# Kernel tuning notes

Hardware: AMD Instinct MI355X
Metric: run time of the kernel (lower is better)

## Reference

```python
import jax, jax.numpy as jnp
import numpy as np

B, T = 16, 4096
H = 1024            # rnn_dims
HALF = H // 2       # half_rnn_dims
FC = 1024           # fc_dims
FEAT, AUX = 80, 64
NC = 256            # n_classes
D_IN = FEAT + AUX + 3


def setup_inputs() -> dict:
    key = jax.random.key(0)
    ks = jax.random.split(key, 20)
    s = 0.02
    inp = {
        "x": jax.random.normal(ks[0], (B, T, 3), jnp.float32),
        "feat": jax.random.normal(ks[1], (B, T, FEAT), jnp.float32),
        "aux1": jax.random.normal(ks[2], (B, T, AUX), jnp.float32),
        "aux2": jax.random.normal(ks[3], (B, T, AUX), jnp.float32),
        "aux3": jax.random.normal(ks[4], (B, T, AUX), jnp.float32),
        # GRU parameters (PyTorch layout: [3*H, in] with r,z,n gate order)
        "w_ih": jax.random.normal(ks[5], (3 * H, D_IN), jnp.float32) * s,
        "w_hh": jax.random.normal(ks[6], (3 * H, H), jnp.float32) * s,
        "b_ih": jax.random.normal(ks[7], (3 * H,), jnp.float32) * s,
        "b_hh": jax.random.normal(ks[8], (3 * H,), jnp.float32) * s,
        # coarse head
        "w1": jax.random.normal(ks[9], (FC, HALF + AUX), jnp.float32) * s,
        "b1": jax.random.normal(ks[10], (FC,), jnp.float32) * s,
        "w2": jax.random.normal(ks[11], (NC, FC), jnp.float32) * s,
        "b2": jax.random.normal(ks[12], (NC,), jnp.float32) * s,
        # fine head
        "w3": jax.random.normal(ks[13], (FC, HALF + AUX), jnp.float32) * s,
        "b3": jax.random.normal(ks[14], (FC,), jnp.float32) * s,
        "w4": jax.random.normal(ks[15], (NC, FC), jnp.float32) * s,
        "b4": jax.random.normal(ks[16], (NC,), jnp.float32) * s,
    }
    return inp


def _gru(inp_btd, w_ih, w_hh, b_ih, b_hh):
    # Precompute input projection for all timesteps: [B,T,3H]
    xp = jnp.einsum("btd,gd->btg", inp_btd, w_ih) + b_ih
    xp = jnp.transpose(xp, (1, 0, 2))  # [T,B,3H]
    h0 = jnp.zeros((inp_btd.shape[0], H), inp_btd.dtype)

    def step(h, xt):
        gh = h @ w_hh.T + b_hh                      # [B,3H]
        xr, xz, xn = jnp.split(xt, 3, axis=1)
        hr, hz, hn = jnp.split(gh, 3, axis=1)
        r = jax.nn.sigmoid(xr + hr)
        z = jax.nn.sigmoid(xz + hz)
        n = jnp.tanh(xn + r * hn)
        h_new = (1.0 - z) * n + z * h
        return h_new, h_new

    _, hs = jax.lax.scan(step, h0, xp)              # [T,B,H]
    return jnp.transpose(hs, (1, 0, 2))             # [B,T,H]


def reference(x, feat, aux1, aux2, aux3, w_ih, w_hh, b_ih, b_hh,
              w1, b1, w2, b2, w3, b3, w4, b4):
    inp = jnp.concatenate([feat, aux1, x], axis=2)  # [B,T,FEAT+AUX+3]
    h = _gru(inp, w_ih, w_hh, b_ih, b_hh)           # [B,T,H]
    h_c, h_f = h[..., :HALF], h[..., HALF:]
    o_c = jax.nn.relu(jnp.concatenate([h_c, aux2], axis=2) @ w1.T + b1)
    p_c = jax.nn.log_softmax(o_c @ w2.T + b2, axis=2)
    o_f = jax.nn.relu(jnp.concatenate([h_f, aux3], axis=2) @ w3.T + b3)
    p_f = jax.nn.log_softmax(o_f @ w4.T + b4, axis=2)
    return (p_c, p_f)
```

## Files before the change

kernel.cpp:

```cpp
#include <hip/hip_runtime.h>
#include <hip/hip_bf16.h>

#define TSTEPS 4096
#define BATCH 16
#define HID 1024
#define DIN 147
#define KIN 160
#define KC  (HID + KIN)
#define NWG 64
#define NCLS 256
#define FCN 1024
#define KFC 576

typedef __attribute__((ext_vector_type(8))) short short8;
typedef __attribute__((ext_vector_type(4))) float floatx4;

__device__ __forceinline__ unsigned short f2b(float f) {
  __hip_bfloat16 h = __float2bfloat16(f);
  return *reinterpret_cast<unsigned short*>(&h);
}

#define GLOAD_LDS16(g, l) __builtin_amdgcn_global_load_lds( \
    (const __attribute__((address_space(1))) void*)(g), \
    (__attribute__((address_space(3))) void*)(l), 16, 0, 0)


__global__ void k_pack(const float* __restrict__ x, const float* __restrict__ feat,
                       const float* __restrict__ aux1, const float* __restrict__ aux2,
                       const float* __restrict__ aux3,
                       unsigned short* __restrict__ Xg, unsigned short* __restrict__ H,
                       unsigned short* __restrict__ a2b, unsigned short* __restrict__ a3b,
                       unsigned int* __restrict__ flags) {
  const int t = blockIdx.x;
  const int tid = threadIdx.x;
  for (int i = tid; i < BATCH * KIN; i += 256) {
    int b = i / KIN, k = i - b * KIN;
    float v = 0.f;
    if (k < 80)       v = feat[((size_t)b * TSTEPS + t) * 80 + k];
    else if (k < 144) v = aux1[((size_t)b * TSTEPS + t) * 64 + (k - 80)];
    else if (k < 147) v = x[((size_t)b * TSTEPS + t) * 3 + (k - 144)];
    Xg[((size_t)t * BATCH + b) * KIN + k] = f2b(v);
  }
  for (int i = tid; i < BATCH * 64; i += 256) {
    int b = i >> 6, k = i & 63;
    a2b[(size_t)t * (BATCH * 64) + i] = f2b(aux2[((size_t)b * TSTEPS + t) * 64 + k]);
    a3b[(size_t)t * (BATCH * 64) + i] = f2b(aux3[((size_t)b * TSTEPS + t) * 64 + k]);
  }
  if (t == 0) {
    for (int i = tid; i < BATCH * HID; i += 256) H[i] = 0;
    for (int i = tid; i < TSTEPS; i += 256) flags[i] = 0u;
  }
}

__global__ void k_wconv(const float* __restrict__ w_ih, const float* __restrict__ w_hh,
                        const float* __restrict__ w1, const float* __restrict__ w2,
                        const float* __restrict__ w3, const float* __restrict__ w4,
                        unsigned short* __restrict__ Wc,
                        unsigned short* __restrict__ w1b, unsigned short* __restrict__ w2b,
                        unsigned short* __restrict__ w3b, unsigned short* __restrict__ w4b) {
  const int bid = blockIdx.x, tid = threadIdx.x;
  if (bid < 3072) {
    const int row = bid;
    for (int k = tid; k < KC; k += 256) {
      float v = 0.f;
      if (k < HID) v = w_hh[(size_t)row * HID + k];
      else if (k < HID + DIN) v = w_ih[(size_t)row * DIN + (k - HID)];
      Wc[(size_t)row * KC + k] = f2b(v);
    }
  } else if (bid < 4096) {
    const int row = bid - 3072;
    for (int k = tid; k < KFC; k += 256) w1b[(size_t)row * KFC + k] = f2b(w1[(size_t)row * KFC + k]);
  } else if (bid < 4352) {
    const int row = bid - 4096;
    for (int k = tid; k < FCN; k += 256) w2b[(size_t)row * FCN + k] = f2b(w2[(size_t)row * FCN + k]);
  } else if (bid < 5376) {
    const int row = bid - 4352;
    for (int k = tid; k < KFC; k += 256) w3b[(size_t)row * KFC + k] = f2b(w3[(size_t)row * KFC + k]);
  } else {
    const int row = bid - 5376;
    for (int k = tid; k < FCN; k += 256) w4b[(size_t)row * FCN + k] = f2b(w4[(size_t)row * FCN + k]);
  }
}

__launch_bounds__(192, 1)
__global__ void k_gru(const unsigned short* __restrict__ Wc,
                      const float* __restrict__ b_ih, const float* __restrict__ b_hh,
                      const unsigned short* __restrict__ Xg,
                      unsigned short* __restrict__ H,
                      unsigned int* __restrict__ flags) {
  const int tid  = threadIdx.x;
  const int wg   = blockIdx.x;
  const int wave = tid >> 6;
  const int gate = wave;
  const int lane = tid & 63;
  const int cn   = lane & 15;
  const int quad = lane >> 4;
  const int c0   = wg * 16;
  const int grow = gate * HID + c0 + cn;

  short8 wf[37];
  {
    const short8* wptr = reinterpret_cast<const short8*>(Wc + (size_t)grow * KC);
#pragma unroll
    for (int ks = 0; ks < 37; ks++) wf[ks] = wptr[ks * 4 + quad];
  }
  const float bih = b_ih[grow];
  const float bhh = b_hh[grow];
  const float brz = bih + bhh;

  float hprev[4] = {0.f, 0.f, 0.f, 0.f};

  __shared__ unsigned short lh[16 * 1024];
  __shared__ float lds_z[256];
  __shared__ float lds_hn[256];
  __shared__ float lds_xn[256];
  __shared__ __align__(16) unsigned lds_hout[128];

  const int swz = (cn & 7) << 3;

  for (int t = 0; t < TSTEPS; t++) {
    floatx4 accx = {0.f, 0.f, 0.f, 0.f};
    {
      const short8* xptr = reinterpret_cast<const short8*>(Xg + ((size_t)t * BATCH + cn) * KIN);
      short8 ax[5];
#pragma unroll
      for (int ks = 0; ks < 5; ks++) ax[ks] = xptr[ks * 4 + quad];
#pragma unroll
      for (int ks = 0; ks < 5; ks++)
        accx = __builtin_amdgcn_mfma_f32_16x16x32_bf16(ax[ks], wf[32 + ks], accx, 0, 0, 0);
    }

    if (wave == 1) {
      const unsigned need = (unsigned)t;
      for (;;) {
        unsigned f = __hip_atomic_load(&flags[lane * 4], __ATOMIC_RELAXED,
                                       __HIP_MEMORY_SCOPE_SYSTEM);
        if (__ballot(f >= need) == ~0ull) break;
      }
      const char* Ht = reinterpret_cast<const char*>(H + (size_t)t * BATCH * HID);
      char* lbase = reinterpret_cast<char*>(lh);
#pragma unroll
      for (int i = 0; i < 32; i++) {
        const int d  = (i << 10) + (lane << 4);
        const int r  = d >> 11;
        const int lb = (d & 2047) ^ ((r & 7) << 4);
        const char* g = Ht + ((lb >> 5) << 9) + (r << 5) + (lb & 31);
        GLOAD_LDS16(g, lbase + (i << 10));
      }
      asm volatile("s_waitcnt vmcnt(0)" ::: "memory");
    }
    asm volatile("" ::: "memory");
    __syncthreads();

    floatx4 acc0 = {0.f, 0.f, 0.f, 0.f};
    floatx4 acc1 = {0.f, 0.f, 0.f, 0.f};
    {
      const int rb = cn * 1024;
#pragma unroll
      for (int ks = 0; ks < 32; ks += 2) {
        short8 a0 = *reinterpret_cast<const short8*>(&lh[rb + (((ks    ) * 32 + quad * 8) ^ swz)]);
        short8 a1 = *reinterpret_cast<const short8*>(&lh[rb + (((ks + 1) * 32 + quad * 8) ^ swz)]);
        acc0 = __builtin_amdgcn_mfma_f32_16x16x32_bf16(a0, wf[ks],     acc0, 0, 0, 0);
        acc1 = __builtin_amdgcn_mfma_f32_16x16x32_bf16(a1, wf[ks + 1], acc1, 0, 0, 0);
      }
    }

    float rr[4];
    if (gate == 0) {
#pragma unroll
      for (int j = 0; j < 4; j++) {
        float g = acc0[j] + acc1[j] + accx[j] + brz;
        rr[j] = __builtin_amdgcn_rcpf(1.f + __expf(-g));
      }
    } else if (gate == 1) {
#pragma unroll
      for (int j = 0; j < 4; j++) {
        float g = acc0[j] + acc1[j] + accx[j] + brz;
        lds_z[(quad * 4 + j) * 16 + cn] = __builtin_amdgcn_rcpf(1.f + __expf(-g));
      }
    } else {
#pragma unroll
      for (int j = 0; j < 4; j++) {
        int idx = (quad * 4 + j) * 16 + cn;
        lds_hn[idx] = acc0[j] + acc1[j] + bhh;
        lds_xn[idx] = accx[j] + bih;
      }
    }
    __syncthreads();

    if (gate == 0) {
#pragma unroll
      for (int j = 0; j < 4; j++) {
        int idx = (quad * 4 + j) * 16 + cn;
        float z = lds_z[idx];
        float a = lds_xn[idx] + rr[j] * lds_hn[idx];
        float e2 = __expf(2.f * a);
        float n = 1.f - 2.f * __builtin_amdgcn_rcpf(e2 + 1.f);
        float h = (1.f - z) * n + z * hprev[j];
        hprev[j] = h;
        unsigned hv = (unsigned)f2b(h);
        unsigned pv = __shfl_xor(hv, 1);
        if ((cn & 1) == 0)
          lds_hout[(quad * 4 + j) * 8 + (cn >> 1)] = hv | (pv << 16);
      }
      unsigned long long v8 = reinterpret_cast<unsigned long long*>(lds_hout)[lane];
      unsigned long long* dst =
          reinterpret_cast<unsigned long long*>(H + (size_t)(t + 1) * BATCH * HID + wg * 256) + lane;
      __hip_atomic_store(dst, v8, __ATOMIC_RELAXED, __HIP_MEMORY_SCOPE_SYSTEM);
      asm volatile("s_waitcnt vmcnt(0)" ::: "memory");
      if (lane == 0)
        __hip_atomic_store(&flags[wg * 4], (unsigned)(t + 1), __ATOMIC_RELAXED,
                           __HIP_MEMORY_SCOPE_SYSTEM);
    }
  }
}

__launch_bounds__(256, 2)
__global__ void k_fc(const unsigned short* __restrict__ H,
                     const unsigned short* __restrict__ a2b, const unsigned short* __restrict__ a3b,
                     const unsigned short* __restrict__ w1b, const unsigned short* __restrict__ w2b,
                     const unsigned short* __restrict__ w3b, const unsigned short* __restrict__ w4b,
                     const float* __restrict__ b1, const float* __restrict__ b2,
                     const float* __restrict__ b3, const float* __restrict__ b4,
                     float* __restrict__ out) {
  const int br = blockIdx.x & 1;
  const int t  = blockIdx.x >> 1;
  const unsigned short* wAp = br ? w3b : w1b;
  const unsigned short* wBp = br ? w4b : w2b;
  const float* bA = br ? b3 : b1;
  const float* bB = br ? b4 : b2;
  const unsigned short* aux = br ? a3b : a2b;
  float* outp = out + (size_t)br * BATCH * TSTEPS * NCLS;

  __shared__ __align__(16) unsigned char smemU[16 * 584 * 2];
  __shared__ __align__(16) unsigned short lO[16][1032];
  unsigned short (*lA)[584] = reinterpret_cast<unsigned short(*)[584]>(smemU);
  float (*lZ)[260] = reinterpret_cast<float(*)[260]>(smemU);

  const int tid  = threadIdx.x;
  const int wave = tid >> 6;
  const int lane = tid & 63;
  const int cn   = lane & 15;
  const int quad = lane >> 4;

  {
    const unsigned short* hb = H + (size_t)(t + 1) * BATCH * HID;
    for (int cid = tid; cid < 16 * 72; cid += 256) {
      int r = cid / 72, off = (cid - r * 72) * 8;
      uint4 v;
      if (off < 512)
        v = *reinterpret_cast<const uint4*>(hb + ((size_t)(br * 32 + (off >> 4))) * 256 + r * 16 + (off & 15));
      else
        v = *reinterpret_cast<const uint4*>(aux + ((size_t)t * 16 + r) * 64 + (off - 512));
      *reinterpret_cast<uint4*>(&lA[r][off]) = v;
    }
  }
  __syncthreads();

  {
    short8 af[18];
#pragma unroll
    for (int ks = 0; ks < 18; ks++)
      af[ks] = *reinterpret_cast<const short8*>(&lA[cn][ks * 32 + quad * 8]);

    for (int nt = 0; nt < 16; nt++) {
      const int colg = wave * 256 + nt * 16 + cn;
      const short8* bptr = reinterpret_cast<const short8*>(wAp + (size_t)colg * KFC);
      floatx4 acc = {0.f, 0.f, 0.f, 0.f};
#pragma unroll
      for (int ks = 0; ks < 18; ks++)
        acc = __builtin_amdgcn_mfma_f32_16x16x32_bf16(af[ks], bptr[ks * 4 + quad], acc, 0, 0, 0);
      const float bias = bA[colg];
#pragma unroll
      for (int j = 0; j < 4; j++) {
        float v = acc[j] + bias;
        v = v > 0.f ? v : 0.f;
        lO[quad * 4 + j][colg] = f2b(v);
      }
    }
  }
  __syncthreads();

  {
    short8 of[32];
#pragma unroll
    for (int ks = 0; ks < 32; ks++)
      of[ks] = *reinterpret_cast<const short8*>(&lO[cn][ks * 32 + quad * 8]);

    for (int nt = 0; nt < 4; nt++) {
      const int cls = wave * 64 + nt * 16 + cn;
      const short8* bptr = reinterpret_cast<const short8*>(wBp + (size_t)cls * FCN);
      floatx4 acc = {0.f, 0.f, 0.f, 0.f};
#pragma unroll
      for (int ks = 0; ks < 32; ks++)
        acc = __builtin_amdgcn_mfma_f32_16x16x32_bf16(of[ks], bptr[ks * 4 + quad], acc, 0, 0, 0);
      const float bias = bB[cls];
#pragma unroll
      for (int j = 0; j < 4; j++)
        lZ[quad * 4 + j][cls] = acc[j] + bias;
    }
  }
  __syncthreads();

  {
    const int r = tid >> 4, j = tid & 15;
    float vals[16];
    float m = -3.4e38f;
#pragma unroll
    for (int i = 0; i < 16; i++) {
      float v = lZ[r][j + 16 * i];
      vals[i] = v;
      m = fmaxf(m, v);
    }
#pragma unroll
    for (int s = 8; s > 0; s >>= 1) m = fmaxf(m, __shfl_xor(m, s, 16));
    float ssum = 0.f;
#pragma unroll
    for (int i = 0; i < 16; i++) ssum += __expf(vals[i] - m);
#pragma unroll
    for (int s = 8; s > 0; s >>= 1) ssum += __shfl_xor(ssum, s, 16);
    const float lse = m + __logf(ssum);
    float* orow = outp + ((size_t)r * TSTEPS + t) * NCLS;
#pragma unroll
    for (int i = 0; i < 16; i++) orow[j + 16 * i] = vals[i] - lse;
  }
}

extern "C" void kernel_launch(void* const* d_in, const int* in_sizes, int n_in,
                              void* d_out, int out_size, void* d_ws, size_t ws_size,
                              hipStream_t stream) {
  const float* x    = (const float*)d_in[0];
  const float* feat = (const float*)d_in[1];
  const float* aux1 = (const float*)d_in[2];
  const float* aux2 = (const float*)d_in[3];
  const float* aux3 = (const float*)d_in[4];
  const float* w_ih = (const float*)d_in[5];
  const float* w_hh = (const float*)d_in[6];
  const float* b_ih = (const float*)d_in[7];
  const float* b_hh = (const float*)d_in[8];
  const float* w1   = (const float*)d_in[9];
  const float* b1   = (const float*)d_in[10];
  const float* w2   = (const float*)d_in[11];
  const float* b2   = (const float*)d_in[12];
  const float* w3   = (const float*)d_in[13];
  const float* b3   = (const float*)d_in[14];
  const float* w4   = (const float*)d_in[15];
  const float* b4   = (const float*)d_in[16];
  float* out = (float*)d_out;

  char* p = (char*)d_ws;
  unsigned short* H   = (unsigned short*)p; p += (size_t)(TSTEPS + 1) * BATCH * HID * 2;
  unsigned short* Xg  = (unsigned short*)p; p += (size_t)TSTEPS * BATCH * KIN * 2;
  unsigned int*  flags = (unsigned int*)p;  p += (size_t)TSTEPS * 4;
  unsigned short* Wc  = (unsigned short*)p; p += (size_t)3072 * KC * 2;
  unsigned short* w1b = (unsigned short*)p; p += (size_t)1024 * KFC * 2;
  unsigned short* w2b = (unsigned short*)p; p += (size_t)256 * FCN * 2;
  unsigned short* w3b = (unsigned short*)p; p += (size_t)1024 * KFC * 2;
  unsigned short* w4b = (unsigned short*)p; p += (size_t)256 * FCN * 2;
  unsigned short* a2b = (unsigned short*)p; p += (size_t)TSTEPS * BATCH * 64 * 2;
  unsigned short* a3b = (unsigned short*)p; p += (size_t)TSTEPS * BATCH * 64 * 2;

  if ((size_t)(p - (char*)d_ws) > ws_size) return;

  k_pack<<<TSTEPS, 256, 0, stream>>>(x, feat, aux1, aux2, aux3, Xg, H, a2b, a3b, flags);
  k_wconv<<<5632, 256, 0, stream>>>(w_ih, w_hh, w1, w2, w3, w4, Wc, w1b, w2b, w3b, w4b);
  k_gru<<<NWG, 192, 0, stream>>>(Wc, b_ih, b_hh, Xg, H, flags);
  k_fc<<<TSTEPS * 2, 256, 0, stream>>>(H, a2b, a3b, w1b, w2b, w3b, w4b, b1, b2, b3, b4, out);
}
```

Baseline: 13.81 ms.

## Fuse FC heads into persistent GRU kernel to overlap with recurrence

The FC/log-softmax heads move into the persistent GRU kernel as 160 extra consumer workgroups. Each one polls the per-workgroup step flags and processes timesteps as soon as the hidden state for that step is published, so the head computation overlaps the serial recurrence instead of running afterwards in a separate launch. The flag layout is also compacted from a stride of four to contiguous entries. The risk is that consumer blocks compete with the latency-critical GRU blocks for memory bandwidth and L2, and they rely on all 224 blocks being co-resident.

Result: slower. 15.79 ms (+14.3%).

```diff
diff --git a/kernel.cpp b/kernel.cpp
--- a/kernel.cpp
+++ b/kernel.cpp
@@ -8,6 +8,7 @@
 #define KIN 160
 #define KC  (HID + KIN)
 #define NWG 64
+#define NFC 160
 #define NCLS 256
 #define FCN 1024
 #define KFC 576
@@ -48,7 +49,7 @@
   }
   if (t == 0) {
     for (int i = tid; i < BATCH * HID; i += 256) H[i] = 0;
-    for (int i = tid; i < TSTEPS; i += 256) flags[i] = 0u;
+    for (int i = tid; i < 256; i += 256) flags[i] = 0u;
   }
 }
 
@@ -87,155 +88,14 @@
                       const float* __restrict__ b_ih, const float* __restrict__ b_hh,
                       const unsigned short* __restrict__ Xg,
                       unsigned short* __restrict__ H,
-                      unsigned int* __restrict__ flags) {
-  const int tid  = threadIdx.x;
-  const int wg   = blockIdx.x;
-  const int wave = tid >> 6;
-  const int gate = wave;
-  const int lane = tid & 63;
-  const int cn   = lane & 15;
-  const int quad = lane >> 4;
-  const int c0   = wg * 16;
-  const int grow = gate * HID + c0 + cn;
-
-  short8 wf[37];
-  {
-    const short8* wptr = reinterpret_cast<const short8*>(Wc + (size_t)grow * KC);
-#pragma unroll
-    for (int ks = 0; ks < 37; ks++) wf[ks] = wptr[ks * 4 + quad];
-  }
-  const float bih = b_ih[grow];
-  const float bhh = b_hh[grow];
-  const float brz = bih + bhh;
-
-  float hprev[4] = {0.f, 0.f, 0.f, 0.f};
-
-  __shared__ unsigned short lh[16 * 1024];
-  __shared__ float lds_z[256];
-  __shared__ float lds_hn[256];
-  __shared__ float lds_xn[256];
-  __shared__ __align__(16) unsigned lds_hout[128];
-
-  const int swz = (cn & 7) << 3;
-
-  for (int t = 0; t < TSTEPS; t++) {
-    floatx4 accx = {0.f, 0.f, 0.f, 0.f};
-    {
-      const short8* xptr = reinterpret_cast<const short8*>(Xg + ((size_t)t * BATCH + cn) * KIN);
-      short8 ax[5];
-#pragma unroll
-      for (int ks = 0; ks < 5; ks++) ax[ks] = xptr[ks * 4 + quad];
-#pragma unroll
-      for (int ks = 0; ks < 5; ks++)
-        accx = __builtin_amdgcn_mfma_f32_16x16x32_bf16(ax[ks], wf[32 + ks], accx, 0, 0, 0);
-    }
-
-    if (wave == 1) {
-      const unsigned need = (unsigned)t;
-      for (;;) {
-        unsigned f = __hip_atomic_load(&flags[lane * 4], __ATOMIC_RELAXED,
-                                       __HIP_MEMORY_SCOPE_SYSTEM);
-        if (__ballot(f >= need) == ~0ull) break;
-      }
-      const char* Ht = reinterpret_cast<const char*>(H + (size_t)t * BATCH * HID);
-      char* lbase = reinterpret_cast<char*>(lh);
-#pragma unroll
-      for (int i = 0; i < 32; i++) {
-        const int d  = (i << 10) + (lane << 4);
-        const int r  = d >> 11;
-        const int lb = (d & 2047) ^ ((r & 7) << 4);
-        const char* g = Ht + ((lb >> 5) << 9) + (r << 5) + (lb & 31);
-        GLOAD_LDS16(g, lbase + (i << 10));
-      }
-      asm volatile("s_waitcnt vmcnt(0)" ::: "memory");
-    }
-    asm volatile("" ::: "memory");
-    __syncthreads();
-
-    floatx4 acc0 = {0.f, 0.f, 0.f, 0.f};
-    floatx4 acc1 = {0.f, 0.f, 0.f, 0.f};
-    {
-      const int rb = cn * 1024;
-#pragma unroll
-      for (int ks = 0; ks < 32; ks += 2) {
-        short8 a0 = *reinterpret_cast<const short8*>(&lh[rb + (((ks    ) * 32 + quad * 8) ^ swz)]);
-        short8 a1 = *reinterpret_cast<const short8*>(&lh[rb + (((ks + 1) * 32 + quad * 8) ^ swz)]);
-        acc0 = __builtin_amdgcn_mfma_f32_16x16x32_bf16(a0, wf[ks],     acc0, 0, 0, 0);
-        acc1 = __builtin_amdgcn_mfma_f32_16x16x32_bf16(a1, wf[ks + 1], acc1, 0, 0, 0);
-      }
-    }
-
-    float rr[4];
-    if (gate == 0) {
-#pragma unroll
-      for (int j = 0; j < 4; j++) {
-        float g = acc0[j] + acc1[j] + accx[j] + brz;
-        rr[j] = __builtin_amdgcn_rcpf(1.f + __expf(-g));
-      }
-    } else if (gate == 1) {
-#pragma unroll
-      for (int j = 0; j < 4; j++) {
-        float g = acc0[j] + acc1[j] + accx[j] + brz;
-        lds_z[(quad * 4 + j) * 16 + cn] = __builtin_amdgcn_rcpf(1.f + __expf(-g));
-      }
-    } else {
-#pragma unroll
-      for (int j = 0; j < 4; j++) {
-        int idx = (quad * 4 + j) * 16 + cn;
-        lds_hn[idx] = acc0[j] + acc1[j] + bhh;
-        lds_xn[idx] = accx[j] + bih;
-      }
-    }
-    __syncthreads();
-
-    if (gate == 0) {
-#pragma unroll
-      for (int j = 0; j < 4; j++) {
-        int idx = (quad * 4 + j) * 16 + cn;
-        float z = lds_z[idx];
-        float a = lds_xn[idx] + rr[j] * lds_hn[idx];
-        float e2 = __expf(2.f * a);
-        float n = 1.f - 2.f * __builtin_amdgcn_rcpf(e2 + 1.f);
-        float h = (1.f - z) * n + z * hprev[j];
-        hprev[j] = h;
-        unsigned hv = (unsigned)f2b(h);
-        unsigned pv = __shfl_xor(hv, 1);
-        if ((cn & 1) == 0)
-          lds_hout[(quad * 4 + j) * 8 + (cn >> 1)] = hv | (pv << 16);
-      }
-      unsigned long long v8 = reinterpret_cast<unsigned long long*>(lds_hout)[lane];
-      unsigned long long* dst =
-          reinterpret_cast<unsigned long long*>(H + (size_t)(t + 1) * BATCH * HID + wg * 256) + lane;
-      __hip_atomic_store(dst, v8, __ATOMIC_RELAXED, __HIP_MEMORY_SCOPE_SYSTEM);
-      asm volatile("s_waitcnt vmcnt(0)" ::: "memory");
-      if (lane == 0)
-        __hip_atomic_store(&flags[wg * 4], (unsigned)(t + 1), __ATOMIC_RELAXED,
-                           __HIP_MEMORY_SCOPE_SYSTEM);
-    }
-  }
-}
-
-__launch_bounds__(256, 2)
-__global__ void k_fc(const unsigned short* __restrict__ H,
-                     const unsigned short* __restrict__ a2b, const unsigned short* __restrict__ a3b,
-                     const unsigned short* __restrict__ w1b, const unsigned short* __restrict__ w2b,
-                     const unsigned short* __restrict__ w3b, const unsigned short* __restrict__ w4b,
-                     const float* __restrict__ b1, const float* __restrict__ b2,
-                     const float* __restrict__ b3, const float* __restrict__ b4,
-                     float* __restrict__ out) {
-  const int br = blockIdx.x & 1;
-  const int t  = blockIdx.x >> 1;
-  const unsigned short* wAp = br ? w3b : w1b;
-  const unsigned short* wBp = br ? w4b : w2b;
-  const float* bA = br ? b3 : b1;
-  const float* bB = br ? b4 : b2;
-  const unsigned short* aux = br ? a3b : a2b;
-  float* outp = out + (size_t)br * BATCH * TSTEPS * NCLS;
-
-  __shared__ __align__(16) unsigned char smemU[16 * 584 * 2];
-  __shared__ __align__(16) unsigned short lO[16][1032];
-  unsigned short (*lA)[584] = reinterpret_cast<unsigned short(*)[584]>(smemU);
-  float (*lZ)[260] = reinterpret_cast<float(*)[260]>(smemU);
+                      unsigned int* __restrict__ flags,
+                      const unsigned short* __restrict__ a2b, const unsigned short* __restrict__ a3b,
+                      const unsigned short* __restrict__ w1b, const unsigned short* __restrict__ w2b,
+                      const unsigned short* __restrict__ w3b, const unsigned short* __restrict__ w4b,
+                      const float* __restrict__ b1, const float* __restrict__ b2,
+                      const float* __restrict__ b3, const float* __restrict__ b4,
+                      float* __restrict__ out) {
+  __shared__ __align__(16) unsigned char smem[51712];
 
   const int tid  = threadIdx.x;
   const int wave = tid >> 6;
@@ -243,86 +103,235 @@
   const int cn   = lane & 15;
   const int quad = lane >> 4;
 
-  {
-    const unsigned short* hb = H + (size_t)(t + 1) * BATCH * HID;
-    for (int cid = tid; cid < 16 * 72; cid += 256) {
-      int r = cid / 72, off = (cid - r * 72) * 8;
-      uint4 v;
-      if (off < 512)
-        v = *reinterpret_cast<const uint4*>(hb + ((size_t)(br * 32 + (off >> 4))) * 256 + r * 16 + (off & 15));
-      else
-        v = *reinterpret_cast<const uint4*>(aux + ((size_t)t * 16 + r) * 64 + (off - 512));
-      *reinterpret_cast<uint4*>(&lA[r][off]) = v;
+  if (blockIdx.x < NWG) {
+    const int wg   = blockIdx.x;
+    const int gate = wave;
+    const int grow = gate * HID + wg * 16 + cn;
+
+    unsigned short* lh = reinterpret_cast<unsigned short*>(smem);
+    float* lds_z  = reinterpret_cast<float*>(smem + 32768);
+    float* lds_hn = reinterpret_cast<float*>(smem + 32768 + 1024);
+    float* lds_xn = reinterpret_cast<float*>(smem + 32768 + 2048);
+    unsigned* lds_hout = reinterpret_cast<unsigned*>(smem + 32768 + 3072);
+
+    short8 wf[37];
+    {
+      const short8* wptr = reinterpret_cast<const short8*>(Wc + (size_t)grow * KC);
+#pragma unroll
+      for (int ks = 0; ks < 37; ks++) wf[ks] = wptr[ks * 4 + quad];
     }
-  }
-  __syncthreads();
-
-  {
-    short8 af[18];
-#pragma unroll
-    for (int ks = 0; ks < 18; ks++)
-      af[ks] = *reinterpret_cast<const short8*>(&lA[cn][ks * 32 + quad * 8]);
-
-    for (int nt = 0; nt < 16; nt++) {
-      const int colg = wave * 256 + nt * 16 + cn;
-      const short8* bptr = reinterpret_cast<const short8*>(wAp + (size_t)colg * KFC);
-      floatx4 acc = {0.f, 0.f, 0.f, 0.f};
-#pragma unroll
-      for (int ks = 0; ks < 18; ks++)
-        acc = __builtin_amdgcn_mfma_f32_16x16x32_bf16(af[ks], bptr[ks * 4 + quad], acc, 0, 0, 0);
-      const float bias = bA[colg];
-#pragma unroll
-      for (int j = 0; j < 4; j++) {
-        float v = acc[j] + bias;
-        v = v > 0.f ? v : 0.f;
-        lO[quad * 4 + j][colg] = f2b(v);
+    const float bih = b_ih[grow];
+    const float bhh = b_hh[grow];
+    const float brz = bih + bhh;
+
+    float hprev[4] = {0.f, 0.f, 0.f, 0.f};
+    const int swz = (cn & 7) << 3;
+
+    for (int t = 0; t < TSTEPS; t++) {
+      floatx4 accx = {0.f, 0.f, 0.f, 0.f};
+      {
+        const short8* xptr = reinterpret_cast<const short8*>(Xg + ((size_t)t * BATCH + cn) * KIN);
+        short8 ax[5];
+#pragma unroll
+        for (int ks = 0; ks < 5; ks++) ax[ks] = xptr[ks * 4 + quad];
+#pragma unroll
+        for (int ks = 0; ks < 5; ks++)
+          accx = __builtin_amdgcn_mfma_f32_16x16x32_bf16(ax[ks], wf[32 + ks], accx, 0, 0, 0);
+      }
+
+      if (wave == 1) {
+        const unsigned need = (unsigned)t;
+        for (;;) {
+          unsigned f = __hip_atomic_load(&flags[lane], __ATOMIC_RELAXED,
+                                         __HIP_MEMORY_SCOPE_SYSTEM);
+          if (__ballot(f >= need) == ~0ull) break;
+        }
+        const char* Ht = reinterpret_cast<const char*>(H + (size_t)t * BATCH * HID);
+        char* lbase = reinterpret_cast<char*>(lh);
+#pragma unroll
+        for (int i = 0; i < 32; i++) {
+          const int d  = (i << 10) + (lane << 4);
+          const int r  = d >> 11;
+          const int lb = (d & 2047) ^ ((r & 7) << 4);
+          const char* g = Ht + ((lb >> 5) << 9) + (r << 5) + (lb & 31);
+          GLOAD_LDS16(g, lbase + (i << 10));
+        }
+        asm volatile("s_waitcnt vmcnt(0)" ::: "memory");
+      }
+      asm volatile("" ::: "memory");
+      __syncthreads();
+
+      floatx4 acc0 = {0.f, 0.f, 0.f, 0.f};
+      floatx4 acc1 = {0.f, 0.f, 0.f, 0.f};
+      {
+        const int rb = cn * 1024;
+#pragma unroll
+        for (int ks = 0; ks < 32; ks += 2) {
+          short8 a0 = *reinterpret_cast<const short8*>(&lh[rb + (((ks    ) * 32 + quad * 8) ^ swz)]);
+          short8 a1 = *reinterpret_cast<const short8*>(&lh[rb + (((ks + 1) * 32 + quad * 8) ^ swz)]);
+          acc0 = __builtin_amdgcn_mfma_f32_16x16x32_bf16(a0, wf[ks],     acc0, 0, 0, 0);
+          acc1 = __builtin_amdgcn_mfma_f32_16x16x32_bf16(a1, wf[ks + 1], acc1, 0, 0, 0);
+        }
+      }
+
+      float rr[4];
+      if (gate == 0) {
+#pragma unroll
+        for (int j = 0; j < 4; j++) {
+          float g = acc0[j] + acc1[j] + accx[j] + brz;
+          rr[j] = __builtin_amdgcn_rcpf(1.f + __expf(-g));
+        }
+      } else if (gate == 1) {
+#pragma unroll
+        for (int j = 0; j < 4; j++) {
+          float g = acc0[j] + acc1[j] + accx[j] + brz;
+          lds_z[(quad * 4 + j) * 16 + cn] = __builtin_amdgcn_rcpf(1.f + __expf(-g));
+        }
+      } else {
+#pragma unroll
+        for (int j = 0; j < 4; j++) {
+          int idx = (quad * 4 + j) * 16 + cn;
+          lds_hn[idx] = acc0[j] + acc1[j] + bhh;
+          lds_xn[idx] = accx[j] + bih;
+        }
+      }
+      __syncthreads();
+
+      if (gate == 0) {
+#pragma unroll
+        for (int j = 0; j < 4; j++) {
+          int idx = (quad * 4 + j) * 16 + cn;
+          float z = lds_z[idx];
+          float a = lds_xn[idx] + rr[j] * lds_hn[idx];
+          float e2 = __expf(2.f * a);
+          float n = 1.f - 2.f * __builtin_amdgcn_rcpf(e2 + 1.f);
+          float h = (1.f - z) * n + z * hprev[j];
+          hprev[j] = h;
+          unsigned hv = (unsigned)f2b(h);
+          unsigned pv = __shfl_xor(hv, 1);
+          if ((cn & 1) == 0)
+            lds_hout[(quad * 4 + j) * 8 + (cn >> 1)] = hv | (pv << 16);
+        }
+        unsigned long long v8 = reinterpret_cast<unsigned long long*>(lds_hout)[lane];
+        unsigned long long* dst =
+            reinterpret_cast<unsigned long long*>(H + (size_t)(t + 1) * BATCH * HID + wg * 256) + lane;
+        __hip_atomic_store(dst, v8, __ATOMIC_RELAXED, __HIP_MEMORY_SCOPE_SYSTEM);
+        asm volatile("s_waitcnt vmcnt(0)" ::: "memory");
+        if (lane == 0)
+          __hip_atomic_store(&flags[wg], (unsigned)(t + 1), __ATOMIC_RELAXED,
+                             __HIP_MEMORY_SCOPE_SYSTEM);
       }
     }
-  }
-  __syncthreads();
-
-  {
-    short8 of[32];
-#pragma unroll
-    for (int ks = 0; ks < 32; ks++)
-      of[ks] = *reinterpret_cast<const short8*>(&lO[cn][ks * 32 + quad * 8]);
-
-    for (int nt = 0; nt < 4; nt++) {
-      const int cls = wave * 64 + nt * 16 + cn;
-      const short8* bptr = reinterpret_cast<const short8*>(wBp + (size_t)cls * FCN);
-      floatx4 acc = {0.f, 0.f, 0.f, 0.f};
-#pragma unroll
-      for (int ks = 0; ks < 32; ks++)
-        acc = __builtin_amdgcn_mfma_f32_16x16x32_bf16(of[ks], bptr[ks * 4 + quad], acc, 0, 0, 0);
-      const float bias = bB[cls];
-#pragma unroll
-      for (int j = 0; j < 4; j++)
-        lZ[quad * 4 + j][cls] = acc[j] + bias;
+  } else {
+    const int w = blockIdx.x - NWG;
+    unsigned short (*lA)[584] = reinterpret_cast<unsigned short(*)[584]>(smem);
+    float (*lZ)[260] = reinterpret_cast<float(*)[260]>(smem);
+    unsigned short (*lO)[1032] = reinterpret_cast<unsigned short(*)[1032]>(smem + 18688);
+
+    for (int idx = w; idx < TSTEPS * 2; idx += NFC) {
+      const int t  = idx >> 1;
+      const int br = idx & 1;
+      const unsigned short* wAp = br ? w3b : w1b;
+      const unsigned short* wBp = br ? w4b : w2b;
+      const float* bA = br ? b3 : b1;
+      const float* bB = br ? b4 : b2;
+      const unsigned short* aux = br ? a3b : a2b;
+      float* outp = out + (size_t)br * BATCH * TSTEPS * NCLS;
+
+      if (wave == 0) {
+        const unsigned need = (unsigned)(t + 1);
+        for (;;) {
+          unsigned f = __hip_atomic_load(&flags[lane], __ATOMIC_RELAXED,
+                                         __HIP_MEMORY_SCOPE_SYSTEM);
+          if (__ballot(f >= need) == ~0ull) break;
+          __builtin_amdgcn_s_sleep(32);
+        }
+      }
+      __syncthreads();
+
+      {
+        const unsigned short* hb = H + (size_t)(t + 1) * BATCH * HID;
+        for (int cid = tid; cid < 16 * 72; cid += 192) {
+          int r = cid / 72, off = (cid - r * 72) * 8;
+          uint4 v;
+          if (off < 512)
+            v = *reinterpret_cast<const uint4*>(hb + ((size_t)(br * 32 + (off >> 4))) * 256 + r * 16 + (off & 15));
+          else
+            v = *reinterpret_cast<const uint4*>(aux + ((size_t)t * 16 + r) * 64 + (off - 512));
+          *reinterpret_cast<uint4*>(&lA[r][off]) = v;
+        }
+      }
+      __syncthreads();
+
+      {
+        short8 af[18];
+#pragma unroll
+        for (int ks = 0; ks < 18; ks++)
+          af[ks] = *reinterpret_cast<const short8*>(&lA[cn][ks * 32 + quad * 8]);
+
+        for (int nt = wave; nt < 64; nt += 3) {
+          const int colg = nt * 16 + cn;
+          const short8* bptr = reinterpret_cast<const short8*>(wAp + (size_t)colg * KFC);
+          floatx4 acc = {0.f, 0.f, 0.f, 0.f};
+#pragma unroll
+          for (int ks = 0; ks < 18; ks++)
+            acc = __builtin_amdgcn_mfma_f32_16x16x32_bf16(af[ks], bptr[ks * 4 + quad], acc, 0, 0, 0);
+          const float bias = bA[colg];
+#pragma unroll
+          for (int j = 0; j < 4; j++) {
+            float v = acc[j] + bias;
+            v = v > 0.f ? v : 0.f;
+            lO[quad * 4 + j][colg] = f2b(v);
+          }
+        }
+      }
+      __syncthreads();
+
+      {
+        short8 of[32];
+#pragma unroll
+        for (int ks = 0; ks < 32; ks++)
+          of[ks] = *reinterpret_cast<const short8*>(&lO[cn][ks * 32 + quad * 8]);
+
+        for (int nt = wave; nt < 16; nt += 3) {
+          const int cls = nt * 16 + cn;
+          const short8* bptr = reinterpret_cast<const short8*>(wBp + (size_t)cls * FCN);
+          floatx4 acc = {0.f, 0.f, 0.f, 0.f};
+#pragma unroll
+          for (int ks = 0; ks < 32; ks++)
+            acc = __builtin_amdgcn_mfma_f32_16x16x32_bf16(of[ks], bptr[ks * 4 + quad], acc, 0, 0, 0);
+          const float bias = bB[cls];
+#pragma unroll
+          for (int j = 0; j < 4; j++)
+            lZ[quad * 4 + j][cls] = acc[j] + bias;
+        }
+      }
+      __syncthreads();
+
+      if (tid < 128) {
+        const int r = tid >> 3, j = tid & 7;
+        float vals[32];
+        float m = -3.4e38f;
+#pragma unroll
+        for (int i = 0; i < 32; i++) {
+          float v = lZ[r][j + 8 * i];
+          vals[i] = v;
+          m = fmaxf(m, v);
+        }
+#pragma unroll
+        for (int s = 4; s > 0; s >>= 1) m = fmaxf(m, __shfl_xor(m, s, 8));
+        float ssum = 0.f;
+#pragma unroll
+        for (int i = 0; i < 32; i++) ssum += __expf(vals[i] - m);
+#pragma unroll
+        for (int s = 4; s > 0; s >>= 1) ssum += __shfl_xor(ssum, s, 8);
+        const float lse = m + __logf(ssum);
+        float* orow = outp + ((size_t)r * TSTEPS + t) * NCLS;
+#pragma unroll
+        for (int i = 0; i < 32; i++) orow[j + 8 * i] = vals[i] - lse;
+      }
+      __syncthreads();
     }
-  }
-  __syncthreads();
-
-  {
-    const int r = tid >> 4, j = tid & 15;
-    float vals[16];
-    float m = -3.4e38f;
-#pragma unroll
-    for (int i = 0; i < 16; i++) {
-      float v = lZ[r][j + 16 * i];
-      vals[i] = v;
-      m = fmaxf(m, v);
-    }
-#pragma unroll
-    for (int s = 8; s > 0; s >>= 1) m = fmaxf(m, __shfl_xor(m, s, 16));
-    float ssum = 0.f;
-#pragma unroll
-    for (int i = 0; i < 16; i++) ssum += __expf(vals[i] - m);
-#pragma unroll
-    for (int s = 8; s > 0; s >>= 1) ssum += __shfl_xor(ssum, s, 16);
-    const float lse = m + __logf(ssum);
-    float* orow = outp + ((size_t)r * TSTEPS + t) * NCLS;
-#pragma unroll
-    for (int i = 0; i < 16; i++) orow[j + 16 * i] = vals[i] - lse;
   }
 }
 
@@ -364,6 +373,7 @@
 
   k_pack<<<TSTEPS, 256, 0, stream>>>(x, feat, aux1, aux2, aux3, Xg, H, a2b, a3b, flags);
   k_wconv<<<5632, 256, 0, stream>>>(w_ih, w_hh, w1, w2, w3, w4, Wc, w1b, w2b, w3b, w4b);
-  k_gru<<<NWG, 192, 0, stream>>>(Wc, b_ih, b_hh, Xg, H, flags);
-  k_fc<<<TSTEPS * 2, 256, 0, stream>>>(H, a2b, a3b, w1b, w2b, w3b, w4b, b1, b2, b3, b4, out);
-}
+  k_gru<<<NWG + NFC, 192, 0, stream>>>(Wc, b_ih, b_hh, Xg, H, flags,
+                                       a2b, a3b, w1b, w2b, w3b, w4b,
+                                       b1, b2, b3, b4, out);
+}
```
